# Performance work log

Measured on AMD Instinct MI355X. Metric: run time of the kernel, lower is better.

Reference implementation:

```python
import jax, jax.numpy as jnp
import numpy as np

B, L, H, D = 4096, 256, 32, 2
LOG_PROB_FACTOR = 0.5

def setup_inputs() -> dict:
    key = jax.random.key(0)
    k0, k1, k2, k3 = jax.random.split(key, 4)
    x = jax.random.randint(k0, (B, L), 0, D)  # spin configs in {0,1}
    Wi = jax.random.normal(k1, (D, 4 * H), dtype=jnp.float32) * 0.1   # input kernel (no bias, flax LSTMCell)
    Wh = jax.random.normal(k2, (H, 4 * H), dtype=jnp.float32) * 0.1   # recurrent kernel
    bh = jnp.zeros((4 * H,), dtype=jnp.float32)                        # recurrent bias
    Wo = jax.random.normal(k3, (H, D), dtype=jnp.float32) * 0.1       # output Dense kernel
    bo = jnp.zeros((D,), dtype=jnp.float32)                            # output Dense bias
    return {"x": x, "Wi": Wi, "Wh": Wh, "bh": bh, "Wo": Wo, "bo": bo}

def reference(x, Wi, Wh, bh, Wo, bo):
    # one-hot of spin t-1 (zeros at t=0); log-prob is read out at spin t.
    x_oh = jax.nn.one_hot(x, D, dtype=Wi.dtype)      # [B, L, D]
    xs = jnp.swapaxes(x_oh, 0, 1)                    # [L, B, D] time-major for scan
    c0 = jnp.zeros((x.shape[0], H), Wi.dtype)
    h0 = jnp.zeros((x.shape[0], H), Wi.dtype)
    inp0 = jnp.zeros((x.shape[0], D), Wi.dtype)      # jnp.zeros(inputDim) initial input

    def step(carry, xt):
        c, h, inp = carry
        gates = inp @ Wi + h @ Wh + bh               # [B, 4H]
        i, f, g, o = jnp.split(gates, 4, axis=-1)    # flax LSTMCell gate order i,f,g,o
        c_new = jax.nn.sigmoid(f) * c + jax.nn.sigmoid(i) * jnp.tanh(g)
        h_new = jax.nn.sigmoid(o) * jnp.tanh(c_new)
        out = jax.nn.elu(h_new @ Wo + bo)            # Dense + actFun, [B, D]
        # log(sum(softmax(out) * onehot)) == gathered log_softmax (stable form)
        logp = jnp.sum(jax.nn.log_softmax(out, axis=-1) * xt, axis=-1)  # [B]
        return (c_new, h_new, xt), logp

    _, logps = jax.lax.scan(step, (c0, h0, inp0), xs)  # logps: [L, B]
    return LOG_PROB_FACTOR * jnp.sum(logps, axis=0)    # [B]
```

## Files before the change

### kernel.cpp

```cpp
#include <hip/hip_runtime.h>


typedef __attribute__((ext_vector_type(8))) short bf16x8;
typedef __attribute__((ext_vector_type(4))) float f32x4;

#define LOG2E 1.4426950408889634f
#define LN2   0.6931471805599453f

__device__ __forceinline__ float fexp2(float x) { return __builtin_amdgcn_exp2f(x); }
__device__ __forceinline__ float flog2(float x) { return __builtin_amdgcn_logf(x); }
__device__ __forceinline__ float frcp(float x)  { return __builtin_amdgcn_rcpf(x); }

__device__ __forceinline__ float fsig(float x)   { return frcp(1.f + fexp2(-LOG2E * x)); }
__device__ __forceinline__ float ftanh_(float x) { return 1.f - 2.f * frcp(fexp2(2.f * LOG2E * x) + 1.f); }
__device__ __forceinline__ float felu(float x)   { return x > 0.f ? x : fexp2(LOG2E * x) - 1.f; }

__device__ __forceinline__ unsigned short f2bf(float f) {
    unsigned u = __builtin_bit_cast(unsigned, f);
    u = (u + 0x7FFFu + ((u >> 16) & 1u)) >> 16;
    return (unsigned short)u;
}

constexpr int Bsz = 4096;

__global__ __launch_bounds__(512, 2) void lstm_r10(
    const int*   __restrict__ x,
    const float* __restrict__ Wi,
    const float* __restrict__ Wh,
    const float* __restrict__ bh,
    const float* __restrict__ Wo,
    const float* __restrict__ bo,
    float*       __restrict__ out)
{
    const int tid  = threadIdx.x;
    const int w    = tid >> 6;
    const int lane = tid & 63;
    const int m    = lane & 15;
    const int oct  = lane >> 4;
    const int rot  = w & 3;
    const int half = w >> 2;
    const int b0   = blockIdx.x * 16;

    __shared__ char   spinT[16][260];
    __shared__ float2 Sbuf[256][16];
    __shared__ short  hbuf[2][16][40];
    __shared__ float  red[8][16];

    {
        const int bl = tid >> 5;
        const int c8 = (tid & 31) * 8;
        const int4* src = reinterpret_cast<const int4*>(x + (b0 + bl) * 256 + c8);
        const int4 v0 = src[0], v1 = src[1];
        const int p0 = (v0.x & 1) | ((v0.y & 1) << 8) | ((v0.z & 1) << 16) | ((v0.w & 1) << 24);
        const int p1 = (v1.x & 1) | ((v1.y & 1) << 8) | ((v1.z & 1) << 16) | ((v1.w & 1) << 24);
        *reinterpret_cast<int*>(&spinT[bl][c8])     = p0;
        *reinterpret_cast<int*>(&spinT[bl][c8 + 4]) = p1;
    }

    bf16x8 wfrag[4];
#pragma unroll
    for (int q = 0; q < 4; ++q) {
        const float gs = (q == 2) ? 2.f * LOG2E : -LOG2E;
        const int colg = 32 * q + 16 * half + ((m + rot) & 15);
#pragma unroll
        for (int j = 0; j < 8; ++j)
            wfrag[q][j] = (short)f2bf(gs * Wh[(oct * 8 + j) * 128 + colg]);
    }
    bf16x8 wofragA;
#pragma unroll
    for (int j = 0; j < 8; ++j)
        wofragA[j] = (m < 2) ? (short)f2bf(Wo[(oct * 8 + j) * 2 + m]) : (short)0;

    const int ucell = 4 * oct + rot + 16 * half;
    float bv0[4], bvd[4];
#pragma unroll
    for (int q = 0; q < 4; ++q) {
        const float gs = (q == 2) ? 2.f * LOG2E : -LOG2E;
        const int c0 = 32 * q + ucell;
        bv0[q] = gs * (bh[c0] + Wi[c0]);
        bvd[q] = gs * (Wi[128 + c0] - Wi[c0]);
    }
    const float bo0 = bo[0], bo1 = bo[1];

    float c = fsig(bh[ucell]) * ftanh_(bh[64 + ucell]);
    hbuf[0][m][ucell] = (short)f2bf(fsig(bh[96 + ucell]) * ftanh_(c));
    __syncthreads();

    const f32x4 zero4 = { 0.f, 0.f, 0.f, 0.f };
    f32x4 ccq[4] = { zero4, zero4, zero4, zero4 };

    auto step = [&](const int t, const int rb, const int wb, const float spf) {
        const bf16x8 hfrag =
            *reinterpret_cast<const bf16x8*>(&hbuf[rb][m][8 * oct]);

#pragma unroll
        for (int q = 0; q < 4; ++q) ccq[q][0] = fmaf(spf, bvd[q], bv0[q]);

        f32x4 acc[4];
#pragma unroll
        for (int q = 0; q < 4; ++q)
            acc[q] = __builtin_amdgcn_mfma_f32_16x16x32_bf16(wfrag[q], hfrag, ccq[q], 0, 0, 0);

        if (((t - 1) & 7) == w) {
            const f32x4 hacc =
                __builtin_amdgcn_mfma_f32_16x16x32_bf16(wofragA, hfrag, zero4, 0, 0, 0);
            if (oct == 0) Sbuf[t - 1][m] = make_float2(hacc[0], hacc[1]);
        }

        {
            const float ei = fexp2(acc[0][0]), ef = fexp2(acc[1][0]);
            const float eg = fexp2(acc[2][0]), eo = fexp2(acc[3][0]);
            const float P = (1.f + ei) * (1.f + eg);
            const float Q = 1.f + ef;
            const float R = frcp(P * Q);
            const float gf  = P * R;
            const float igt = (eg - 1.f) * Q * R;
            c = fmaf(gf, c, igt);
            const float ec = fexp2(2.f * LOG2E * c);
            const float h  = (ec - 1.f) * frcp((1.f + eo) * (1.f + ec));
            hbuf[wb][m][ucell] = (short)f2bf(h);
        }
        __syncthreads();
    };

    unsigned sp2 = *reinterpret_cast<const unsigned short*>(&spinT[m][0]);
    for (int tb = 1; tb < 255; tb += 2) {
        const unsigned sp2n =
            *reinterpret_cast<const unsigned short*>(&spinT[m][tb + 1]);
        step(tb,     0, 1, (float)(sp2 & 0xFFu));
        step(tb + 1, 1, 0, (float)(sp2 >> 8));
        sp2 = sp2n;
    }
    step(255, 0, 1, (float)(sp2 & 0xFFu));

    if (w == 7) {
        const bf16x8 hfrag = *reinterpret_cast<const bf16x8*>(&hbuf[1][m][8 * oct]);
        const f32x4 hacc =
            __builtin_amdgcn_mfma_f32_16x16x32_bf16(wofragA, hfrag, zero4, 0, 0, 0);
        if (oct == 0) Sbuf[255][m] = make_float2(hacc[0], hacc[1]);
    }
    __syncthreads();

    float lp = 0.f;
    {
        const int t0 = (w * 4 + oct) * 8;
#pragma unroll
        for (int i = 0; i < 8; ++i) {
            const int t = t0 + i;
            const float2 sv = Sbuf[t][m];
            const int sp = spinT[m][t];
            const float o0 = felu(sv.x + bo0);
            const float o1 = felu(sv.y + bo1);
            const float mx = fmaxf(o0, o1), mn = fminf(o0, o1);
            const float lse = mx + LN2 * flog2(1.f + fexp2(LOG2E * (mn - mx)));
            lp += (sp ? o1 : o0) - lse;
        }
    }
    lp += __shfl_xor(lp, 16, 64);
    lp += __shfl_xor(lp, 32, 64);
    if (lane < 16) red[w][lane] = lp;
    __syncthreads();
    if (tid < 16) {
        float s = 0.f;
#pragma unroll
        for (int ww = 0; ww < 8; ++ww) s += red[ww][tid];
        out[b0 + tid] = 0.5f * s;
    }
}

extern "C" void kernel_launch(void* const* d_in, const int* in_sizes, int n_in,
                              void* d_out, int out_size, void* d_ws, size_t ws_size,
                              hipStream_t stream) {
    const int*   x  = (const int*)d_in[0];
    const float* Wi = (const float*)d_in[1];
    const float* Wh = (const float*)d_in[2];
    const float* bh = (const float*)d_in[3];
    const float* Wo = (const float*)d_in[4];
    const float* bo = (const float*)d_in[5];
    float* out = (float*)d_out;

    lstm_r10<<<dim3(Bsz / 16), dim3(512), 0, stream>>>(x, Wi, Wh, bh, Wo, bo, out);
}
```

Baseline: 136.2 us.

## Split block into two 8-sample groups ping-ponging MFMA and cell phases

Each block's 16 samples are split into two groups of 8, each owned by four waves. While one group runs the recurrent MFMAs, the other runs the elementwise LSTM cell update, alternating between barriers so matrix and transcendental work overlap. The Wo readout is folded into unused rows of the first Wh fragment, which removes the separate output MFMA. Each wave now issues eight MFMAs per step instead of four, with half the columns wasted, and the number of barriers per timestep doubles.

```diff
diff --git a/kernel.cpp b/kernel.cpp
--- a/kernel.cpp
+++ b/kernel.cpp
@@ -23,7 +23,7 @@
 
 constexpr int Bsz = 4096;
 
-__global__ __launch_bounds__(512, 2) void lstm_r10(
+__global__ __launch_bounds__(512, 2) void lstm_r11(
     const int*   __restrict__ x,
     const float* __restrict__ Wi,
     const float* __restrict__ Wh,
@@ -38,12 +38,14 @@
     const int m    = lane & 15;
     const int oct  = lane >> 4;
     const int rot  = w & 3;
-    const int half = w >> 2;
+    const int grp  = w >> 2;
+    const int mlo  = m & 7;
+    const int mhi  = m >> 3;
     const int b0   = blockIdx.x * 16;
 
     __shared__ char   spinT[16][260];
     __shared__ float2 Sbuf[256][16];
-    __shared__ short  hbuf[2][16][40];
+    __shared__ short  hbuf[2][8][40];
     __shared__ float  red[8][16];
 
     {
@@ -57,21 +59,24 @@
         *reinterpret_cast<int*>(&spinT[bl][c8 + 4]) = p1;
     }
 
-    bf16x8 wfrag[4];
+    bf16x8 wfrag[4][2];
 #pragma unroll
     for (int q = 0; q < 4; ++q) {
         const float gs = (q == 2) ? 2.f * LOG2E : -LOG2E;
-        const int colg = 32 * q + 16 * half + ((m + rot) & 15);
 #pragma unroll
-        for (int j = 0; j < 8; ++j)
-            wfrag[q][j] = (short)f2bf(gs * Wh[(oct * 8 + j) * 128 + colg]);
+        for (int hh = 0; hh < 2; ++hh) {
+            const int colg = 32 * q + 16 * hh + ((m + rot) & 15);
+#pragma unroll
+            for (int j = 0; j < 8; ++j) {
+                float v = gs * Wh[(oct * 8 + j) * 128 + colg];
+                if (q == 0 && hh == 0 && m == 1) v = Wo[(oct * 8 + j) * 2 + 0];
+                if (q == 0 && hh == 0 && m == 2) v = Wo[(oct * 8 + j) * 2 + 1];
+                wfrag[q][hh][j] = (short)f2bf(v);
+            }
+        }
     }
-    bf16x8 wofragA;
-#pragma unroll
-    for (int j = 0; j < 8; ++j)
-        wofragA[j] = (m < 2) ? (short)f2bf(Wo[(oct * 8 + j) * 2 + m]) : (short)0;
 
-    const int ucell = 4 * oct + rot + 16 * half;
+    const int ucell = 4 * oct + rot + 16 * mhi;
     float bv0[4], bvd[4];
 #pragma unroll
     for (int q = 0; q < 4; ++q) {
@@ -83,61 +88,65 @@
     const float bo0 = bo[0], bo1 = bo[1];
 
     float c = fsig(bh[ucell]) * ftanh_(bh[64 + ucell]);
-    hbuf[0][m][ucell] = (short)f2bf(fsig(bh[96 + ucell]) * ftanh_(c));
+    hbuf[grp][mlo][ucell] = (short)f2bf(fsig(bh[96 + ucell]) * ftanh_(c));
     __syncthreads();
 
+    const int grpS = __builtin_amdgcn_readfirstlane(grp);
+    const int rotS = __builtin_amdgcn_readfirstlane(rot);
     const f32x4 zero4 = { 0.f, 0.f, 0.f, 0.f };
-    f32x4 ccq[4] = { zero4, zero4, zero4, zero4 };
+    f32x4 accq[4][2];
+    int spn = 0;
 
-    auto step = [&](const int t, const int rb, const int wb, const float spf) {
-        const bf16x8 hfrag =
-            *reinterpret_cast<const bf16x8*>(&hbuf[rb][m][8 * oct]);
+    const short* hrd = &hbuf[grp][mlo][8 * oct];
+    short*       hwr = &hbuf[grp][mlo][ucell];
+    const char*  srd = &spinT[grp * 8 + mlo][0];
 
-#pragma unroll
-        for (int q = 0; q < 4; ++q) ccq[q][0] = fmaf(spf, bvd[q], bv0[q]);
-
-        f32x4 acc[4];
+    auto MEM = [&](const int tr) {
+        const bf16x8 hfrag = *reinterpret_cast<const bf16x8*>(hrd);
+        spn = (int)srd[tr];
 #pragma unroll
         for (int q = 0; q < 4; ++q)
-            acc[q] = __builtin_amdgcn_mfma_f32_16x16x32_bf16(wfrag[q], hfrag, ccq[q], 0, 0, 0);
-
-        if (((t - 1) & 7) == w) {
-            const f32x4 hacc =
-                __builtin_amdgcn_mfma_f32_16x16x32_bf16(wofragA, hfrag, zero4, 0, 0, 0);
-            if (oct == 0) Sbuf[t - 1][m] = make_float2(hacc[0], hacc[1]);
+#pragma unroll
+            for (int hh = 0; hh < 2; ++hh)
+                accq[q][hh] = __builtin_amdgcn_mfma_f32_16x16x32_bf16(
+                    wfrag[q][hh], hfrag, zero4, 0, 0, 0);
+        if (rotS == (tr & 3)) {
+            if (oct == 0 && m < 8)
+                Sbuf[tr][grp * 8 + m] = make_float2(accq[0][0][1], accq[0][0][2]);
         }
-
-        {
-            const float ei = fexp2(acc[0][0]), ef = fexp2(acc[1][0]);
-            const float eg = fexp2(acc[2][0]), eo = fexp2(acc[3][0]);
-            const float P = (1.f + ei) * (1.f + eg);
-            const float Q = 1.f + ef;
-            const float R = frcp(P * Q);
-            const float gf  = P * R;
-            const float igt = (eg - 1.f) * Q * R;
-            c = fmaf(gf, c, igt);
-            const float ec = fexp2(2.f * LOG2E * c);
-            const float h  = (ec - 1.f) * frcp((1.f + eo) * (1.f + ec));
-            hbuf[wb][m][ucell] = (short)f2bf(h);
-        }
-        __syncthreads();
     };
 
-    unsigned sp2 = *reinterpret_cast<const unsigned short*>(&spinT[m][0]);
-    for (int tb = 1; tb < 255; tb += 2) {
-        const unsigned sp2n =
-            *reinterpret_cast<const unsigned short*>(&spinT[m][tb + 1]);
-        step(tb,     0, 1, (float)(sp2 & 0xFFu));
-        step(tb + 1, 1, 0, (float)(sp2 >> 8));
-        sp2 = sp2n;
+    auto CELL = [&]() {
+        const float spf = (float)spn;
+        const float a0 = fmaf(spf, bvd[0], bv0[0]) + (mhi ? accq[0][1][0] : accq[0][0][0]);
+        const float a1 = fmaf(spf, bvd[1], bv0[1]) + (mhi ? accq[1][1][0] : accq[1][0][0]);
+        const float a2 = fmaf(spf, bvd[2], bv0[2]) + (mhi ? accq[2][1][0] : accq[2][0][0]);
+        const float a3 = fmaf(spf, bvd[3], bv0[3]) + (mhi ? accq[3][1][0] : accq[3][0][0]);
+        const float ei = fexp2(a0), ef = fexp2(a1);
+        const float eg = fexp2(a2), eo = fexp2(a3);
+        const float P = (1.f + ei) * (1.f + eg);
+        const float Q = 1.f + ef;
+        const float R = frcp(P * Q);
+        const float gf  = P * R;
+        const float igt = (eg - 1.f) * Q * R;
+        c = fmaf(gf, c, igt);
+        const float ec = fexp2(2.f * LOG2E * c);
+        const float h  = (ec - 1.f) * frcp((1.f + eo) * (1.f + ec));
+        *hwr = (short)f2bf(h);
+    };
+
+    if (grpS != 0) MEM(0);
+    for (int j = 0; j < 255; ++j) {
+        if (grpS == 0) MEM(j); else CELL();
+        __syncthreads();
+        if (grpS == 0) CELL(); else MEM(j + 1);
+        __syncthreads();
     }
-    step(255, 0, 1, (float)(sp2 & 0xFFu));
-
-    if (w == 7) {
-        const bf16x8 hfrag = *reinterpret_cast<const bf16x8*>(&hbuf[1][m][8 * oct]);
-        const f32x4 hacc =
-            __builtin_amdgcn_mfma_f32_16x16x32_bf16(wofragA, hfrag, zero4, 0, 0, 0);
-        if (oct == 0) Sbuf[255][m] = make_float2(hacc[0], hacc[1]);
+    if (grpS == 0 && rotS == 0) {
+        const bf16x8 hfrag = *reinterpret_cast<const bf16x8*>(hrd);
+        const f32x4 hs = __builtin_amdgcn_mfma_f32_16x16x32_bf16(
+            wfrag[0][0], hfrag, zero4, 0, 0, 0);
+        if (oct == 0 && m < 8) Sbuf[255][m] = make_float2(hs[1], hs[2]);
     }
     __syncthreads();
 
@@ -179,5 +188,5 @@
     const float* bo = (const float*)d_in[5];
     float* out = (float*)d_out;
 
-    lstm_r10<<<dim3(Bsz / 16), dim3(512), 0, stream>>>(x, Wi, Wh, bh, Wo, bo, out);
+    lstm_r11<<<dim3(Bsz / 16), dim3(512), 0, stream>>>(x, Wi, Wh, bh, Wo, bo, out);
 }
```

Measured after the change: 183.1 us. 34.4% more time.

## Halve batch rows per block, fold output projection into gate MFMA

Applied to the files above, without the earlier changes.

Each block now handles 8 batch rows with 4 waves instead of 16 rows with 8 waves, which doubles the grid to 512 blocks. The MFMA output rows are repacked so one 16x16 tile holds two gate columns for the 8 rows plus the two Wo output columns. This removes the separate output-projection MFMA, and the bias is added after the MFMA instead of seeded into the accumulator. The aim is more blocks for better CU coverage and a lighter per-step barrier across 4 waves. The cost is that half of each MFMA tile is wasted and a 36000-byte dynamic shared allocation is requested without being used, which may limit occupancy.

```diff
diff --git a/kernel.cpp b/kernel.cpp
--- a/kernel.cpp
+++ b/kernel.cpp
@@ -23,7 +23,7 @@
 
 constexpr int Bsz = 4096;
 
-__global__ __launch_bounds__(512, 2) void lstm_r10(
+__global__ __launch_bounds__(256, 2) void lstm_r12(
     const int*   __restrict__ x,
     const float* __restrict__ Wi,
     const float* __restrict__ Wh,
@@ -37,14 +37,15 @@
     const int lane = tid & 63;
     const int m    = lane & 15;
     const int oct  = lane >> 4;
-    const int rot  = w & 3;
-    const int half = w >> 2;
-    const int b0   = blockIdx.x * 16;
+    const int rot  = w;
+    const int mb   = m & 7;
+    const int hi   = m >> 3;
+    const int b0   = blockIdx.x * 8;
 
-    __shared__ char   spinT[16][260];
-    __shared__ float2 Sbuf[256][16];
-    __shared__ short  hbuf[2][16][40];
-    __shared__ float  red[8][16];
+    __shared__ char   spinT[8][260];
+    __shared__ float2 Sbuf[256][8];
+    __shared__ short  hbuf[2][8][40];
+    __shared__ float  red[4][8];
 
     {
         const int bl = tid >> 5;
@@ -61,17 +62,17 @@
 #pragma unroll
     for (int q = 0; q < 4; ++q) {
         const float gs = (q == 2) ? 2.f * LOG2E : -LOG2E;
-        const int colg = 32 * q + 16 * half + ((m + rot) & 15);
+        const int r = m & 3, a = m >> 2;
 #pragma unroll
-        for (int j = 0; j < 8; ++j)
-            wfrag[q][j] = (short)f2bf(gs * Wh[(oct * 8 + j) * 128 + colg]);
+        for (int j = 0; j < 8; ++j) {
+            float v = 0.f;
+            if (r < 2)          v = gs * Wh[(oct * 8 + j) * 128 + (32 * q + 16 * r + 4 * a + rot)];
+            else if (q == 0)    v = Wo[(oct * 8 + j) * 2 + (r - 2)];
+            wfrag[q][j] = (short)f2bf(v);
+        }
     }
-    bf16x8 wofragA;
-#pragma unroll
-    for (int j = 0; j < 8; ++j)
-        wofragA[j] = (m < 2) ? (short)f2bf(Wo[(oct * 8 + j) * 2 + m]) : (short)0;
 
-    const int ucell = 4 * oct + rot + 16 * half;
+    const int ucell = 4 * oct + rot + 16 * hi;
     float bv0[4], bvd[4];
 #pragma unroll
     for (int q = 0; q < 4; ++q) {
@@ -83,72 +84,78 @@
     const float bo0 = bo[0], bo1 = bo[1];
 
     float c = fsig(bh[ucell]) * ftanh_(bh[64 + ucell]);
-    hbuf[0][m][ucell] = (short)f2bf(fsig(bh[96 + ucell]) * ftanh_(c));
+    hbuf[0][mb][ucell] = (short)f2bf(fsig(bh[96 + ucell]) * ftanh_(c));
     __syncthreads();
 
+    const int rotS = __builtin_amdgcn_readfirstlane(rot);
     const f32x4 zero4 = { 0.f, 0.f, 0.f, 0.f };
-    f32x4 ccq[4] = { zero4, zero4, zero4, zero4 };
+
+    const short* hrd = &hbuf[0][mb][8 * oct];
+    const int    hstride = 8 * 40;
 
     auto step = [&](const int t, const int rb, const int wb, const float spf) {
         const bf16x8 hfrag =
-            *reinterpret_cast<const bf16x8*>(&hbuf[rb][m][8 * oct]);
-
-#pragma unroll
-        for (int q = 0; q < 4; ++q) ccq[q][0] = fmaf(spf, bvd[q], bv0[q]);
+            *reinterpret_cast<const bf16x8*>(&hbuf[rb][mb][8 * oct]);
 
         f32x4 acc[4];
 #pragma unroll
         for (int q = 0; q < 4; ++q)
-            acc[q] = __builtin_amdgcn_mfma_f32_16x16x32_bf16(wfrag[q], hfrag, ccq[q], 0, 0, 0);
+            acc[q] = __builtin_amdgcn_mfma_f32_16x16x32_bf16(wfrag[q], hfrag, zero4, 0, 0, 0);
 
-        if (((t - 1) & 7) == w) {
-            const f32x4 hacc =
-                __builtin_amdgcn_mfma_f32_16x16x32_bf16(wofragA, hfrag, zero4, 0, 0, 0);
-            if (oct == 0) Sbuf[t - 1][m] = make_float2(hacc[0], hacc[1]);
+        if (rotS == ((t - 1) & 3)) {
+            if (oct == 0 && m < 8)
+                Sbuf[t - 1][m] = make_float2(acc[0][2], acc[0][3]);
         }
 
-        {
-            const float ei = fexp2(acc[0][0]), ef = fexp2(acc[1][0]);
-            const float eg = fexp2(acc[2][0]), eo = fexp2(acc[3][0]);
-            const float P = (1.f + ei) * (1.f + eg);
-            const float Q = 1.f + ef;
-            const float R = frcp(P * Q);
-            const float gf  = P * R;
-            const float igt = (eg - 1.f) * Q * R;
-            c = fmaf(gf, c, igt);
-            const float ec = fexp2(2.f * LOG2E * c);
-            const float h  = (ec - 1.f) * frcp((1.f + eo) * (1.f + ec));
-            hbuf[wb][m][ucell] = (short)f2bf(h);
-        }
+        const float g0 = hi ? acc[0][1] : acc[0][0];
+        const float g1 = hi ? acc[1][1] : acc[1][0];
+        const float g2 = hi ? acc[2][1] : acc[2][0];
+        const float g3 = hi ? acc[3][1] : acc[3][0];
+
+        const float a0 = fmaf(spf, bvd[0], bv0[0]) + g0;
+        const float a1 = fmaf(spf, bvd[1], bv0[1]) + g1;
+        const float a2 = fmaf(spf, bvd[2], bv0[2]) + g2;
+        const float a3 = fmaf(spf, bvd[3], bv0[3]) + g3;
+        const float ei = fexp2(a0), ef = fexp2(a1);
+        const float eg = fexp2(a2), eo = fexp2(a3);
+        const float P = (1.f + ei) * (1.f + eg);
+        const float Q = 1.f + ef;
+        const float R = frcp(P * Q);
+        const float gf  = P * R;
+        const float igt = (eg - 1.f) * Q * R;
+        c = fmaf(gf, c, igt);
+        const float ec = fexp2(2.f * LOG2E * c);
+        const float h  = (ec - 1.f) * frcp((1.f + eo) * (1.f + ec));
+        hbuf[wb][mb][ucell] = (short)f2bf(h);
         __syncthreads();
     };
 
-    unsigned sp2 = *reinterpret_cast<const unsigned short*>(&spinT[m][0]);
+    unsigned sp2 = *reinterpret_cast<const unsigned short*>(&spinT[mb][0]);
     for (int tb = 1; tb < 255; tb += 2) {
         const unsigned sp2n =
-            *reinterpret_cast<const unsigned short*>(&spinT[m][tb + 1]);
+            *reinterpret_cast<const unsigned short*>(&spinT[mb][tb + 1]);
         step(tb,     0, 1, (float)(sp2 & 0xFFu));
         step(tb + 1, 1, 0, (float)(sp2 >> 8));
         sp2 = sp2n;
     }
     step(255, 0, 1, (float)(sp2 & 0xFFu));
 
-    if (w == 7) {
-        const bf16x8 hfrag = *reinterpret_cast<const bf16x8*>(&hbuf[1][m][8 * oct]);
-        const f32x4 hacc =
-            __builtin_amdgcn_mfma_f32_16x16x32_bf16(wofragA, hfrag, zero4, 0, 0, 0);
-        if (oct == 0) Sbuf[255][m] = make_float2(hacc[0], hacc[1]);
+    if (rotS == 0) {
+        const bf16x8 hfrag = *reinterpret_cast<const bf16x8*>(&hbuf[1][mb][8 * oct]);
+        const f32x4 hs =
+            __builtin_amdgcn_mfma_f32_16x16x32_bf16(wfrag[0], hfrag, zero4, 0, 0, 0);
+        if (oct == 0 && m < 8) Sbuf[255][m] = make_float2(hs[2], hs[3]);
     }
     __syncthreads();
 
     float lp = 0.f;
     {
-        const int t0 = (w * 4 + oct) * 8;
+        const int t0 = ((w * 4 + oct) * 2 + hi) * 8;
 #pragma unroll
         for (int i = 0; i < 8; ++i) {
             const int t = t0 + i;
-            const float2 sv = Sbuf[t][m];
-            const int sp = spinT[m][t];
+            const float2 sv = Sbuf[t][mb];
+            const int sp = spinT[mb][t];
             const float o0 = felu(sv.x + bo0);
             const float o1 = felu(sv.y + bo1);
             const float mx = fmaxf(o0, o1), mn = fminf(o0, o1);
@@ -158,14 +165,16 @@
     }
     lp += __shfl_xor(lp, 16, 64);
     lp += __shfl_xor(lp, 32, 64);
-    if (lane < 16) red[w][lane] = lp;
+    lp += __shfl_xor(lp, 8, 64);
+    if (lane < 8) red[w][lane] = lp;
     __syncthreads();
-    if (tid < 16) {
+    if (tid < 8) {
         float s = 0.f;
 #pragma unroll
-        for (int ww = 0; ww < 8; ++ww) s += red[ww][tid];
+        for (int ww = 0; ww < 4; ++ww) s += red[ww][tid];
         out[b0 + tid] = 0.5f * s;
     }
+    (void)hrd; (void)hstride;
 }
 
 extern "C" void kernel_launch(void* const* d_in, const int* in_sizes, int n_in,
@@ -179,5 +188,5 @@
     const float* bo = (const float*)d_in[5];
     float* out = (float*)d_out;
 
-    lstm_r10<<<dim3(Bsz / 16), dim3(512), 0, stream>>>(x, Wi, Wh, bh, Wo, bo, out);
+    lstm_r12<<<dim3(Bsz / 8), dim3(256), 36000, stream>>>(x, Wi, Wh, bh, Wo, bo, out);
 }
```

Result: no change. 134.5 us (-1.2%).

## Keep each wave's 4 batch rows in-register, exchange hidden state via bpermute

Applied to the files above, without the earlier changes.

Restructures the recurrence so each of 4 waves owns 4 batch elements and computes all 128 gate columns itself with 8 MFMAs per step. The hidden state is redistributed within the wave using ds_bpermute and byte permutes instead of a shared-memory buffer, which removes the per-step __syncthreads across 8 waves. In exchange each wave issues twice as many MFMAs per step and each lane updates two cells. The block shrinks to 256 threads with a different launch-bounds occupancy hint.

```diff
diff --git a/kernel.cpp b/kernel.cpp
--- a/kernel.cpp
+++ b/kernel.cpp
@@ -3,6 +3,7 @@
 
 typedef __attribute__((ext_vector_type(8))) short bf16x8;
 typedef __attribute__((ext_vector_type(4))) float f32x4;
+typedef __attribute__((ext_vector_type(4))) unsigned int u32x4;
 
 #define LOG2E 1.4426950408889634f
 #define LN2   0.6931471805599453f
@@ -23,7 +24,7 @@
 
 constexpr int Bsz = 4096;
 
-__global__ __launch_bounds__(512, 2) void lstm_r10(
+__global__ __launch_bounds__(256, 1) void lstm_r13(
     const int*   __restrict__ x,
     const float* __restrict__ Wi,
     const float* __restrict__ Wh,
@@ -33,137 +34,180 @@
     float*       __restrict__ out)
 {
     const int tid  = threadIdx.x;
-    const int w    = tid >> 6;
+    const int wv   = tid >> 6;
     const int lane = tid & 63;
     const int m    = lane & 15;
     const int oct  = lane >> 4;
-    const int rot  = w & 3;
-    const int half = w >> 2;
+    const int g    = (m >> 2) & 3;
+    const int b    = m & 3;
+    const int mb   = 4 * wv + b;
     const int b0   = blockIdx.x * 16;
 
     __shared__ char   spinT[16][260];
     __shared__ float2 Sbuf[256][16];
-    __shared__ short  hbuf[2][16][40];
-    __shared__ float  red[8][16];
-
-    {
-        const int bl = tid >> 5;
-        const int c8 = (tid & 31) * 8;
-        const int4* src = reinterpret_cast<const int4*>(x + (b0 + bl) * 256 + c8);
-        const int4 v0 = src[0], v1 = src[1];
-        const int p0 = (v0.x & 1) | ((v0.y & 1) << 8) | ((v0.z & 1) << 16) | ((v0.w & 1) << 24);
-        const int p1 = (v1.x & 1) | ((v1.y & 1) << 8) | ((v1.z & 1) << 16) | ((v1.w & 1) << 24);
-        *reinterpret_cast<int*>(&spinT[bl][c8])     = p0;
-        *reinterpret_cast<int*>(&spinT[bl][c8 + 4]) = p1;
-    }
-
-    bf16x8 wfrag[4];
-#pragma unroll
-    for (int q = 0; q < 4; ++q) {
-        const float gs = (q == 2) ? 2.f * LOG2E : -LOG2E;
-        const int colg = 32 * q + 16 * half + ((m + rot) & 15);
-#pragma unroll
-        for (int j = 0; j < 8; ++j)
-            wfrag[q][j] = (short)f2bf(gs * Wh[(oct * 8 + j) * 128 + colg]);
-    }
-    bf16x8 wofragA;
+    __shared__ float  red[16][16];
+
+    {
+        const int bl  = tid >> 4;
+        const int c16 = (tid & 15) * 16;
+        const int4* src = reinterpret_cast<const int4*>(x + (b0 + bl) * 256 + c16);
+#pragma unroll
+        for (int q = 0; q < 4; ++q) {
+            const int4 v = src[q];
+            const int pk = (v.x & 1) | ((v.y & 1) << 8) | ((v.z & 1) << 16) | ((v.w & 1) << 24);
+            *reinterpret_cast<int*>(&spinT[bl][c16 + 4 * q]) = pk;
+        }
+    }
+
+    bf16x8 wfrag[8];
+    {
+        const int qa = m & 3, ua = m >> 2;
+        const float gsq = (qa == 2) ? 2.f * LOG2E : -LOG2E;
+#pragma unroll
+        for (int t8 = 0; t8 < 8; ++t8) {
+            const int colg = 32 * qa + 4 * t8 + ua;
+#pragma unroll
+            for (int j = 0; j < 8; ++j)
+                wfrag[t8][j] = (short)f2bf(gsq * Wh[(8 * oct + j) * 128 + colg]);
+        }
+    }
+    bf16x8 wfragO;
 #pragma unroll
     for (int j = 0; j < 8; ++j)
-        wofragA[j] = (m < 2) ? (short)f2bf(Wo[(oct * 8 + j) * 2 + m]) : (short)0;
-
-    const int ucell = 4 * oct + rot + 16 * half;
-    float bv0[4], bvd[4];
-#pragma unroll
-    for (int q = 0; q < 4; ++q) {
-        const float gs = (q == 2) ? 2.f * LOG2E : -LOG2E;
-        const int c0 = 32 * q + ucell;
-        bv0[q] = gs * (bh[c0] + Wi[c0]);
-        bvd[q] = gs * (Wi[128 + c0] - Wi[c0]);
+        wfragO[j] = (m < 2) ? (short)f2bf(Wo[(8 * oct + j) * 2 + m]) : (short)0;
+
+    const int u1 = 8 * g + oct, u2 = u1 + 4;
+    float bv00[4], bvd0[4], bv01[4], bvd1[4];
+#pragma unroll
+    for (int r = 0; r < 4; ++r) {
+        const float gsr = (r == 2) ? 2.f * LOG2E : -LOG2E;
+        const int cA = 32 * r + u1, cB = 32 * r + u2;
+        bv00[r] = gsr * (bh[cA] + Wi[cA]); bvd0[r] = gsr * (Wi[128 + cA] - Wi[cA]);
+        bv01[r] = gsr * (bh[cB] + Wi[cB]); bvd1[r] = gsr * (Wi[128 + cB] - Wi[cB]);
     }
     const float bo0 = bo[0], bo1 = bo[1];
 
-    float c = fsig(bh[ucell]) * ftanh_(bh[64 + ucell]);
-    hbuf[0][m][ucell] = (short)f2bf(fsig(bh[96 + ucell]) * ftanh_(c));
+    const int ad0 = 4 * ((0 << 4) | (oct << 2) | b);
+    const int ad1 = 4 * ((1 << 4) | (oct << 2) | b);
+    const int ad2 = 4 * ((2 << 4) | (oct << 2) | b);
+    const int ad3 = 4 * ((3 << 4) | (oct << 2) | b);
+
     __syncthreads();
 
+    float c1 = fsig(bh[u1]) * ftanh_(bh[64 + u1]);
+    float c2 = fsig(bh[u2]) * ftanh_(bh[64 + u2]);
+    unsigned p = (unsigned)f2bf(fsig(bh[96 + u1]) * ftanh_(c1))
+               | ((unsigned)f2bf(fsig(bh[96 + u2]) * ftanh_(c2)) << 16);
+
     const f32x4 zero4 = { 0.f, 0.f, 0.f, 0.f };
-    f32x4 ccq[4] = { zero4, zero4, zero4, zero4 };
-
-    auto step = [&](const int t, const int rb, const int wb, const float spf) {
-        const bf16x8 hfrag =
-            *reinterpret_cast<const bf16x8*>(&hbuf[rb][m][8 * oct]);
-
-#pragma unroll
-        for (int q = 0; q < 4; ++q) ccq[q][0] = fmaf(spf, bvd[q], bv0[q]);
-
-        f32x4 acc[4];
-#pragma unroll
-        for (int q = 0; q < 4; ++q)
-            acc[q] = __builtin_amdgcn_mfma_f32_16x16x32_bf16(wfrag[q], hfrag, ccq[q], 0, 0, 0);
-
-        if (((t - 1) & 7) == w) {
-            const f32x4 hacc =
-                __builtin_amdgcn_mfma_f32_16x16x32_bf16(wofragA, hfrag, zero4, 0, 0, 0);
-            if (oct == 0) Sbuf[t - 1][m] = make_float2(hacc[0], hacc[1]);
-        }
-
-        {
-            const float ei = fexp2(acc[0][0]), ef = fexp2(acc[1][0]);
-            const float eg = fexp2(acc[2][0]), eo = fexp2(acc[3][0]);
-            const float P = (1.f + ei) * (1.f + eg);
-            const float Q = 1.f + ef;
-            const float R = frcp(P * Q);
-            const float gf  = P * R;
-            const float igt = (eg - 1.f) * Q * R;
-            c = fmaf(gf, c, igt);
-            const float ec = fexp2(2.f * LOG2E * c);
-            const float h  = (ec - 1.f) * frcp((1.f + eo) * (1.f + ec));
-            hbuf[wb][m][ucell] = (short)f2bf(h);
-        }
-        __syncthreads();
+
+    auto cellup = [](float a0, float a1, float a2, float a3, float& cc) -> float {
+        const float ei = fexp2(a0), ef = fexp2(a1);
+        const float eg = fexp2(a2), eo = fexp2(a3);
+        const float P = (1.f + ei) * (1.f + eg);
+        const float Q = 1.f + ef;
+        const float R = frcp(P * Q);
+        cc = fmaf(P * R, cc, (eg - 1.f) * Q * R);
+        const float ec = fexp2(2.f * LOG2E * cc);
+        return (ec - 1.f) * frcp((1.f + eo) * (1.f + ec));
     };
 
-    unsigned sp2 = *reinterpret_cast<const unsigned short*>(&spinT[m][0]);
+    auto step = [&](const int t, const float spf) {
+        const int P0 = __builtin_amdgcn_ds_bpermute(ad0, (int)p);
+        const int P1 = __builtin_amdgcn_ds_bpermute(ad1, (int)p);
+        const int P2 = __builtin_amdgcn_ds_bpermute(ad2, (int)p);
+        const int P3 = __builtin_amdgcn_ds_bpermute(ad3, (int)p);
+
+        f32x4 cb0, cb1;
+#pragma unroll
+        for (int r = 0; r < 4; ++r) {
+            cb0[r] = fmaf(spf, bvd0[r], bv00[r]);
+            cb1[r] = fmaf(spf, bvd1[r], bv01[r]);
+        }
+
+        const unsigned d0 = __builtin_amdgcn_perm((unsigned)P1, (unsigned)P0, 0x05040100u);
+        const unsigned d1 = __builtin_amdgcn_perm((unsigned)P3, (unsigned)P2, 0x05040100u);
+        const unsigned d2 = __builtin_amdgcn_perm((unsigned)P1, (unsigned)P0, 0x07060302u);
+        const unsigned d3 = __builtin_amdgcn_perm((unsigned)P3, (unsigned)P2, 0x07060302u);
+        u32x4 hv; hv[0] = d0; hv[1] = d1; hv[2] = d2; hv[3] = d3;
+        const bf16x8 hfrag = __builtin_bit_cast(bf16x8, hv);
+
+        f32x4 aq[8];
+#pragma unroll
+        for (int t8 = 0; t8 < 8; ++t8)
+            aq[t8] = __builtin_amdgcn_mfma_f32_16x16x32_bf16(
+                wfrag[t8], hfrag, (t8 & 1) ? cb1 : cb0, 0, 0, 0);
+        const f32x4 accO = __builtin_amdgcn_mfma_f32_16x16x32_bf16(
+            wfragO, hfrag, zero4, 0, 0, 0);
+        if (oct == 0 && m < 4)
+            Sbuf[t - 1][4 * wv + m] = make_float2(accO[0], accO[1]);
+
+        const bool gb0 = (g & 1), gb1_ = (g & 2);
+        float ge[4], go_[4];
+#pragma unroll
+        for (int r = 0; r < 4; ++r) {
+            const float eA = gb1_ ? aq[4][r] : aq[0][r];
+            const float eB = gb1_ ? aq[6][r] : aq[2][r];
+            ge[r] = gb0 ? eB : eA;
+            const float oA = gb1_ ? aq[5][r] : aq[1][r];
+            const float oB = gb1_ ? aq[7][r] : aq[3][r];
+            go_[r] = gb0 ? oB : oA;
+        }
+        const float h1 = cellup(ge[0],  ge[1],  ge[2],  ge[3],  c1);
+        const float h2 = cellup(go_[0], go_[1], go_[2], go_[3], c2);
+        p = (unsigned)f2bf(h1) | ((unsigned)f2bf(h2) << 16);
+    };
+
+    unsigned sp2 = *reinterpret_cast<const unsigned short*>(&spinT[mb][0]);
     for (int tb = 1; tb < 255; tb += 2) {
         const unsigned sp2n =
-            *reinterpret_cast<const unsigned short*>(&spinT[m][tb + 1]);
-        step(tb,     0, 1, (float)(sp2 & 0xFFu));
-        step(tb + 1, 1, 0, (float)(sp2 >> 8));
+            *reinterpret_cast<const unsigned short*>(&spinT[mb][tb + 1]);
+        step(tb,     (float)(sp2 & 0xFFu));
+        step(tb + 1, (float)(sp2 >> 8));
         sp2 = sp2n;
     }
-    step(255, 0, 1, (float)(sp2 & 0xFFu));
-
-    if (w == 7) {
-        const bf16x8 hfrag = *reinterpret_cast<const bf16x8*>(&hbuf[1][m][8 * oct]);
-        const f32x4 hacc =
-            __builtin_amdgcn_mfma_f32_16x16x32_bf16(wofragA, hfrag, zero4, 0, 0, 0);
-        if (oct == 0) Sbuf[255][m] = make_float2(hacc[0], hacc[1]);
+    step(255, (float)(sp2 & 0xFFu));
+
+    {
+        const int P0 = __builtin_amdgcn_ds_bpermute(ad0, (int)p);
+        const int P1 = __builtin_amdgcn_ds_bpermute(ad1, (int)p);
+        const int P2 = __builtin_amdgcn_ds_bpermute(ad2, (int)p);
+        const int P3 = __builtin_amdgcn_ds_bpermute(ad3, (int)p);
+        const unsigned d0 = __builtin_amdgcn_perm((unsigned)P1, (unsigned)P0, 0x05040100u);
+        const unsigned d1 = __builtin_amdgcn_perm((unsigned)P3, (unsigned)P2, 0x05040100u);
+        const unsigned d2 = __builtin_amdgcn_perm((unsigned)P1, (unsigned)P0, 0x07060302u);
+        const unsigned d3 = __builtin_amdgcn_perm((unsigned)P3, (unsigned)P2, 0x07060302u);
+        u32x4 hv; hv[0] = d0; hv[1] = d1; hv[2] = d2; hv[3] = d3;
+        const bf16x8 hfrag = __builtin_bit_cast(bf16x8, hv);
+        const f32x4 accO = __builtin_amdgcn_mfma_f32_16x16x32_bf16(
+            wfragO, hfrag, zero4, 0, 0, 0);
+        if (oct == 0 && m < 4)
+            Sbuf[255][4 * wv + m] = make_float2(accO[0], accO[1]);
     }
     __syncthreads();
 
     float lp = 0.f;
     {
-        const int t0 = (w * 4 + oct) * 8;
-#pragma unroll
-        for (int i = 0; i < 8; ++i) {
-            const int t = t0 + i;
-            const float2 sv = Sbuf[t][m];
-            const int sp = spinT[m][t];
+        const int bpost = tid & 15;
+        const int tc    = tid >> 4;
+#pragma unroll
+        for (int i = 0; i < 16; ++i) {
+            const int t = tc * 16 + i;
+            const float2 sv = Sbuf[t][bpost];
+            const int sp = spinT[bpost][t];
             const float o0 = felu(sv.x + bo0);
             const float o1 = felu(sv.y + bo1);
             const float mx = fmaxf(o0, o1), mn = fminf(o0, o1);
             const float lse = mx + LN2 * flog2(1.f + fexp2(LOG2E * (mn - mx)));
             lp += (sp ? o1 : o0) - lse;
         }
-    }
-    lp += __shfl_xor(lp, 16, 64);
-    lp += __shfl_xor(lp, 32, 64);
-    if (lane < 16) red[w][lane] = lp;
+        red[tc][bpost] = lp;
+    }
     __syncthreads();
     if (tid < 16) {
         float s = 0.f;
 #pragma unroll
-        for (int ww = 0; ww < 8; ++ww) s += red[ww][tid];
+        for (int tc2 = 0; tc2 < 16; ++tc2) s += red[tc2][tid];
         out[b0 + tid] = 0.5f * s;
     }
 }
@@ -179,5 +223,5 @@
     const float* bo = (const float*)d_in[5];
     float* out = (float*)d_out;
 
-    lstm_r10<<<dim3(Bsz / 16), dim3(512), 0, stream>>>(x, Wi, Wh, bh, Wo, bo, out);
+    lstm_r13<<<dim3(Bsz / 16), dim3(256), 0, stream>>>(x, Wi, Wh, bh, Wo, bo, out);
 }
```

New measurement: 161.0 us. 18.3% more time.
